# Kernel optimization log

Hardware: AMD Instinct MI355X
Metric: run time of the kernel (lower is better)

The kernel has to match this reference:

```python
import jax, jax.numpy as jnp
import numpy as np

B, T, D, S, K = 8, 4096, 1024, 64, 3
EPS = 1e-5

def setup_inputs() -> dict:
    key = jax.random.key(0)
    ks = jax.random.split(key, 10)
    def lin(k, out_d, in_d):
        s = 1.0 / np.sqrt(in_d)
        return jax.random.uniform(k, (out_d, in_d), jnp.float32, -s, s)
    return {
        "x": jax.random.normal(ks[0], (B, T, D), jnp.float32),
        "norm_w": jnp.ones((D,), jnp.float32),
        "norm_b": jnp.zeros((D,), jnp.float32),
        "in_w": lin(ks[1], 2 * D, D),
        "in_b": jnp.zeros((2 * D,), jnp.float32),
        "conv_w": jax.random.normal(ks[2], (D, 1, K), jnp.float32) / np.sqrt(K),
        "conv_b": jnp.zeros((D,), jnp.float32),
        "dt_w": lin(ks[3], S, D),
        "dt_b": jnp.zeros((S,), jnp.float32),
        "b_w": lin(ks[4], S, D),
        "b_b": jnp.zeros((S,), jnp.float32),
        "c_w": lin(ks[5], S, D),
        "c_b": jnp.zeros((S,), jnp.float32),
        "a_log": jax.random.normal(ks[6], (S,), jnp.float32) * 0.02,
        "d": jnp.ones((D,), jnp.float32),
        "out_w": lin(ks[7], D, D + S),
        "out_b": jnp.zeros((D,), jnp.float32),
    }

def reference(x, norm_w, norm_b, in_w, in_b, conv_w, conv_b,
              dt_w, dt_b, b_w, b_b, c_w, c_b, a_log, d, out_w, out_b):
    bsz, tlen, dim = x.shape
    sdim = a_log.shape[0]
    k = conv_w.shape[-1]
    residual = x
    # LayerNorm
    mu = jnp.mean(x, axis=-1, keepdims=True)
    var = jnp.mean(jnp.square(x - mu), axis=-1, keepdims=True)
    xn = (x - mu) * jax.lax.rsqrt(var + EPS) * norm_w + norm_b
    # in_proj and chunk
    h = xn @ in_w.T + in_b                       # (B,T,2D)
    x_proj, z = jnp.split(h, 2, axis=-1)         # each (B,T,D)
    # depthwise conv over time, 'same' padding
    xc = jax.lax.conv_general_dilated(
        x_proj.transpose(0, 2, 1), conv_w, (1,), [(k // 2, k // 2)],
        dimension_numbers=("NCH", "OIH", "NCH"), feature_group_count=dim)
    x_conv = jnp.tanh((xc + conv_b[None, :, None]).transpose(0, 2, 1))  # (B,T,D)
    # gate projections for all timesteps at once
    dt = jax.nn.softplus(z @ dt_w.T + dt_b) + 1e-4   # (B,T,S)
    b = jnp.tanh(z @ b_w.T + b_b)                    # (B,T,S)
    c = jnp.tanh(z @ c_w.T + c_b)                    # (B,T,S)
    a = -jnp.exp(a_log)                              # (S,)
    decay = jnp.exp(a * dt)                          # (B,T,S)
    # linear recurrence: state_t = state_{t-1} * decay_t + b_t
    def step(state, inp):
        dec_t, b_t = inp
        state = state * dec_t + b_t
        return state, state
    _, states = jax.lax.scan(step, jnp.zeros((bsz, sdim), x.dtype),
                             (decay.transpose(1, 0, 2), b.transpose(1, 0, 2)))
    states = states.transpose(1, 0, 2)               # (B,T,S)
    y = c * states
    mix = jnp.concatenate([x_conv * d, y], axis=-1)  # (B,T,D+S)
    out = mix @ out_w.T + out_b                      # (B,T,D)
    return residual + out
```

## Files before the change

kernel.cpp:

```cpp
#include <hip/hip_runtime.h>

#define TT 4096
#define DD 1024
#define NN 32768

typedef short s16x8 __attribute__((ext_vector_type(8)));
typedef float f32x4 __attribute__((ext_vector_type(4)));
typedef unsigned short ushort_t;

__device__ __forceinline__ unsigned short f2bf(float f) {
  unsigned u = __float_as_uint(f);
  u += 0x7FFFu + ((u >> 16) & 1u);
  return (unsigned short)(u >> 16);
}
__device__ __forceinline__ float bf2f(unsigned short h) {
  return __uint_as_float(((unsigned)h) << 16);
}
__device__ __forceinline__ void load_lds16(const void* g, void* l) {
  __builtin_amdgcn_global_load_lds(
      (const __attribute__((address_space(1))) unsigned int*)g,
      (__attribute__((address_space(3))) unsigned int*)l, 16, 0, 0);
}

__global__ __launch_bounds__(256)
void cvt_kernel(const float* __restrict__ s, ushort_t* __restrict__ d, int n) {
  int i = (blockIdx.x * 256 + threadIdx.x) * 4;
  if (i < n) {
    float4 v = *(const float4*)&s[i];
    ushort4 o; o.x = f2bf(v.x); o.y = f2bf(v.y); o.z = f2bf(v.z); o.w = f2bf(v.w);
    *(ushort4*)&d[i] = o;
  }
}

__global__ __launch_bounds__(256)
void w3pad_kernel(const float* __restrict__ dt_w, const float* __restrict__ b_w,
                  const float* __restrict__ c_w, ushort_t* __restrict__ w3) {
  int e = (blockIdx.x * 256 + threadIdx.x) * 4;
  int row = e >> 10, col = e & 1023;
  float4 v; v.x = 0.f; v.y = 0.f; v.z = 0.f; v.w = 0.f;
  if (row < 64)       v = *(const float4*)&dt_w[(row << 10) + col];
  else if (row < 128) v = *(const float4*)&b_w[((row - 64) << 10) + col];
  else if (row < 192) v = *(const float4*)&c_w[((row - 128) << 10) + col];
  ushort4 o; o.x = f2bf(v.x); o.y = f2bf(v.y); o.z = f2bf(v.z); o.w = f2bf(v.w);
  *(ushort4*)&w3[e] = o;
}

__global__ __launch_bounds__(256)
void ln_kernel(const float* __restrict__ x, const float* __restrict__ w,
               const float* __restrict__ bv, ushort_t* __restrict__ xn)
{
  int row = blockIdx.x * 4 + (threadIdx.x >> 6);
  int lane = threadIdx.x & 63;
  const float* xr = x + (size_t)row * DD;
  float4 v[4];
  float s = 0.f, ss = 0.f;
  #pragma unroll
  for (int j = 0; j < 4; ++j) {
    v[j] = *(const float4*)&xr[j * 256 + lane * 4];
    s  += v[j].x + v[j].y + v[j].z + v[j].w;
    ss += v[j].x * v[j].x + v[j].y * v[j].y + v[j].z * v[j].z + v[j].w * v[j].w;
  }
  #pragma unroll
  for (int off = 32; off > 0; off >>= 1) {
    s  += __shfl_xor(s, off, 64);
    ss += __shfl_xor(ss, off, 64);
  }
  float mean = s * (1.f / 1024.f);
  float var  = ss * (1.f / 1024.f) - mean * mean;
  float rinv = rsqrtf(var + 1e-5f);
  #pragma unroll
  for (int j = 0; j < 4; ++j) {
    int c = j * 256 + lane * 4;
    float4 wv = *(const float4*)&w[c];
    float4 bb = *(const float4*)&bv[c];
    ushort4 o;
    o.x = f2bf((v[j].x - mean) * rinv * wv.x + bb.x);
    o.y = f2bf((v[j].y - mean) * rinv * wv.y + bb.y);
    o.z = f2bf((v[j].z - mean) * rinv * wv.z + bb.z);
    o.w = f2bf((v[j].w - mean) * rinv * wv.w + bb.w);
    *(ushort4*)&xn[(size_t)row * DD + c] = o;
  }
}

template<int EP>
__global__ __launch_bounds__(512, 2)
void gemm256(const ushort_t* __restrict__ A, const ushort_t* __restrict__ W,
             int M, int N, int K,
             const float* __restrict__ bias0,
             ushort_t* __restrict__ o0, ushort_t* __restrict__ o1)
{
  __shared__ ushort_t lds[65536];
  const int tid = threadIdx.x;
  const int lane = tid & 63;
  const int wid = tid >> 6;
  const int wr = wid >> 2;
  const int wc = wid & 3;
  const int lane15 = lane & 15;
  const int lgrp = lane >> 4;
  const int rsw = (lane15 & 7) << 4;
  const int ntn = N >> 8;
  int bid = blockIdx.x;
  { const int cpx = (int)gridDim.x >> 3; bid = (bid & 7) * cpx + (bid >> 3); }
  const int brow = (bid / ntn) << 8;
  const int bcol = (bid % ntn) << 8;
  const int nk = K >> 6;
  const int sRow = tid >> 3;
  const int sCol = (tid & 7) << 4;
  const char* ldsb = (const char*)lds;
  (void)M;

#define STG(bufb, isB, h, kt) do { \
    const int ktc_ = (kt) < nk ? (kt) : nk - 1; \
    const ushort_t* gsrc_ = (isB) ? W : A; \
    const int rowb_ = ((isB) ? bcol : brow) + (h) * 128; \
    _Pragma("unroll") \
    for (int j_ = 0; j_ < 2; ++j_) { \
      const int r_ = j_ * 64 + sRow; \
      load_lds16((const char*)(gsrc_ + (size_t)(rowb_ + r_) * K) + ktc_ * 128 + (sCol ^ ((r_ & 7) << 4)), \
                 (char*)lds + (bufb) * 65536 + (isB) * 32768 + (h) * 16384 + r_ * 128 + sCol); \
    } } while (0)

#define LDA_(bufb, m, kk) \
  (*(const s16x8*)(ldsb + (bufb) * 65536 + wr * 16384 + ((m) * 16 + lane15) * 128 + (((kk) * 64 + lgrp * 16) ^ rsw)))
#define LDB_(bufb, n, kk) \
  (*(const s16x8*)(ldsb + (bufb) * 65536 + 32768 + (wc >> 1) * 16384 + ((wc & 1) * 64 + (n) * 16 + lane15) * 128 + (((kk) * 64 + lgrp * 16) ^ rsw)))

#define BARR() asm volatile("s_barrier" ::: "memory")
#define VMW2() asm volatile("s_waitcnt vmcnt(2)" ::: "memory")
#define VMW4() asm volatile("s_waitcnt vmcnt(4)" ::: "memory")

#define RDA(dst, bufb, mh) do { \
    _Pragma("unroll") for (int kk = 0; kk < 2; ++kk) \
    _Pragma("unroll") for (int q = 0; q < 4; ++q) \
      dst[kk][q] = LDA_(bufb, (mh) * 4 + q, kk); } while (0)
#define RDB(dst, bufb, nh) do { \
    _Pragma("unroll") for (int kk = 0; kk < 2; ++kk) \
    _Pragma("unroll") for (int p = 0; p < 2; ++p) \
      dst[kk][p] = LDB_(bufb, (nh) * 2 + p, kk); } while (0)

#define MFMAQ(AF, BF, mh, nh) do { \
    __builtin_amdgcn_s_setprio(1); \
    _Pragma("unroll") for (int kk = 0; kk < 2; ++kk) \
    _Pragma("unroll") for (int q = 0; q < 4; ++q) \
    _Pragma("unroll") for (int p = 0; p < 2; ++p) \
      acc[(mh) * 4 + q][(nh) * 2 + p] = __builtin_amdgcn_mfma_f32_16x16x32_bf16( \
          AF[kk][q], BF[kk][p], acc[(mh) * 4 + q][(nh) * 2 + p], 0, 0, 0); \
    __builtin_amdgcn_s_setprio(0); } while (0)

  f32x4 acc[8][4];
  #pragma unroll
  for (int m = 0; m < 8; ++m) {
    #pragma unroll
    for (int n = 0; n < 4; ++n) acc[m][n] = (f32x4){0.f, 0.f, 0.f, 0.f};
  }
  s16x8 afP[2][4], afQ[2][4];
  s16x8 b0[2][2], b1[2][2];

  STG(0, 1, 0, 0); STG(0, 0, 0, 0); STG(0, 0, 1, 0); STG(0, 1, 1, 0);
  STG(1, 1, 0, 1); STG(1, 0, 0, 1);
  VMW4(); BARR();
  RDA(afP, 0, 0); RDB(b0, 0, 0);

  const int nIter = nk >> 1;
  for (int it = 0; it < nIter; ++it) {
    const int t0 = 2 * it;
    STG(1, 0, 1, t0 + 1);
    MFMAQ(afP, b0, 0, 0);
    RDB(b1, 0, 1); BARR();
    STG(1, 1, 1, t0 + 1);
    MFMAQ(afP, b1, 0, 1);
    RDA(afQ, 0, 1); BARR();
    STG(0, 1, 0, t0 + 2);
    MFMAQ(afQ, b1, 1, 1);
    VMW2(); BARR();
    STG(0, 0, 0, t0 + 2);
    MFMAQ(afQ, b0, 1, 0);
    RDA(afP, 1, 0); RDB(b1, 1, 1); BARR();
    STG(0, 0, 1, t0 + 2);
    MFMAQ(afP, b1, 0, 1);
    RDB(b0, 1, 0); BARR();
    STG(0, 1, 1, t0 + 2);
    MFMAQ(afP, b0, 0, 0);
    RDA(afQ, 1, 1); BARR();
    STG(1, 1, 0, t0 + 3);
    MFMAQ(afQ, b0, 1, 0);
    VMW2(); BARR();
    STG(1, 0, 0, t0 + 3);
    MFMAQ(afQ, b1, 1, 1);
    RDA(afP, 0, 0); RDB(b0, 0, 0); BARR();
  }
  if (nk & 1) {
    MFMAQ(afP, b0, 0, 0);
    RDB(b1, 0, 1);
    MFMAQ(afP, b1, 0, 1);
    RDA(afQ, 0, 1);
    MFMAQ(afQ, b1, 1, 1);
    MFMAQ(afQ, b0, 1, 0);
  }

#undef STG
#undef LDA_
#undef LDB_
#undef BARR
#undef VMW2
#undef VMW4
#undef RDA
#undef RDB
#undef MFMAQ

  #pragma unroll
  for (int m = 0; m < 8; ++m) {
    #pragma unroll
    for (int i = 0; i < 4; ++i) {
      const int r = brow + wr * 128 + m * 16 + lgrp * 4 + i;
      #pragma unroll
      for (int n = 0; n < 4; ++n) {
        const int col = bcol + wc * 64 + n * 16 + lane15;
        float v = acc[m][n][i] + bias0[col];
        if (col < DD) o0[(size_t)r * DD + col] = f2bf(v);
        else          o1[(size_t)r * DD + (col - DD)] = f2bf(v);
      }
    }
  }
}

__global__ __launch_bounds__(512, 4)
void gemm3_bk32(const ushort_t* __restrict__ A, const ushort_t* __restrict__ W,
                int M, int N, int K,
                const float* __restrict__ bias, const float* __restrict__ resid,
                float* __restrict__ outf)
{
  __shared__ ushort_t lds[24576];
  const int tid = threadIdx.x;
  const int lane = tid & 63;
  const int wid = tid >> 6;
  const int wr = wid >> 2;
  const int wc = wid & 3;
  const int lane15 = lane & 15;
  const int lgrp = lane >> 4;
  const int ntn = N >> 8;
  int bid = blockIdx.x;
  { const int cpx = (int)gridDim.x >> 3; bid = (bid & 7) * cpx + (bid >> 3); }
  const int brow = (bid / ntn) << 7;
  const int bcol = (bid % ntn) << 8;
  const int nk = K >> 5;
  const int sR = tid >> 2;
  const int sC = (tid & 3) << 4;
  const char* ldsb = (const char*)lds;
  (void)M;

  f32x4 acc[4][4];
  #pragma unroll
  for (int q = 0; q < 4; ++q)
    #pragma unroll
    for (int p = 0; p < 4; ++p) acc[q][p] = (f32x4){0.f, 0.f, 0.f, 0.f};

#define STG3(bufb, kt) do { \
    load_lds16((const char*)(A + (size_t)(brow + sR) * K + (kt) * 32) + sC, \
               (char*)lds + (bufb) * 24576 + sR * 64 + sC); \
    load_lds16((const char*)(W + (size_t)(bcol + sR) * K + (kt) * 32) + sC, \
               (char*)lds + (bufb) * 24576 + 8192 + sR * 64 + sC); \
    load_lds16((const char*)(W + (size_t)(bcol + 128 + sR) * K + (kt) * 32) + sC, \
               (char*)lds + (bufb) * 24576 + 8192 + (128 + sR) * 64 + sC); \
  } while (0)

  STG3(0, 0);
  __syncthreads();

  int cur = 0;
  for (int t = 0; t < nk; ++t) {
    if (t + 1 < nk) STG3(cur ^ 1, t + 1);
    s16x8 af[4], bf[4];
    #pragma unroll
    for (int q = 0; q < 4; ++q)
      af[q] = *(const s16x8*)(ldsb + cur * 24576 + (wr * 64 + q * 16 + lane15) * 64 + lgrp * 16);
    #pragma unroll
    for (int p = 0; p < 4; ++p)
      bf[p] = *(const s16x8*)(ldsb + cur * 24576 + 8192 + (wc * 64 + p * 16 + lane15) * 64 + lgrp * 16);
    __builtin_amdgcn_s_setprio(1);
    #pragma unroll
    for (int q = 0; q < 4; ++q)
      #pragma unroll
      for (int p = 0; p < 4; ++p)
        acc[q][p] = __builtin_amdgcn_mfma_f32_16x16x32_bf16(af[q], bf[p], acc[q][p], 0, 0, 0);
    __builtin_amdgcn_s_setprio(0);
    __syncthreads();
    cur ^= 1;
  }
#undef STG3

  #pragma unroll
  for (int q = 0; q < 4; ++q) {
    #pragma unroll
    for (int i = 0; i < 4; ++i) {
      const int r = brow + wr * 64 + q * 16 + lgrp * 4 + i;
      #pragma unroll
      for (int p = 0; p < 4; ++p) {
        const int col = bcol + wc * 64 + p * 16 + lane15;
        outf[(size_t)r * DD + col] = acc[q][p][i] + bias[col] + resid[(size_t)r * DD + col];
      }
    }
  }
}

__global__ __launch_bounds__(256)
void gemm128(const ushort_t* __restrict__ A, const ushort_t* __restrict__ W,
             int M, int N, int K,
             const float* __restrict__ bias0, const float* __restrict__ bias1,
             const float* __restrict__ bias2, const float* __restrict__ alog,
             float* __restrict__ g0, float* __restrict__ g1, float* __restrict__ g2)
{
  __shared__ ushort_t As[128 * 64];
  __shared__ ushort_t Bs[128 * 64];
  const int tid = threadIdx.x;
  const int lane = tid & 63;
  const int wid = tid >> 6;
  const int ntn = N >> 7;
  const int brow = (blockIdx.x / ntn) << 7;
  const int bcol = (blockIdx.x % ntn) << 7;
  const int wr = (wid >> 1) << 6;
  const int wc = (wid & 1) << 6;
  const int lane15 = lane & 15;
  const int lgrp = lane >> 4;
  (void)M;

  f32x4 acc[4][4];
  #pragma unroll
  for (int m = 0; m < 4; ++m)
    #pragma unroll
    for (int n = 0; n < 4; ++n)
      acc[m][n] = (f32x4){0.f, 0.f, 0.f, 0.f};

  const int r0 = tid >> 3;
  const int c0 = (tid & 7) << 3;
  const ushort_t* gA = A + (size_t)(brow + r0) * K + c0;
  const ushort_t* gW = W + (size_t)(bcol + r0) * K + c0;
  ushort_t* lA = &As[r0 * 64 + c0];
  ushort_t* lB = &Bs[r0 * 64 + c0];

  for (int k0 = 0; k0 < K; k0 += 64) {
    #pragma unroll
    for (int j = 0; j < 4; ++j) {
      load_lds16(gA + (size_t)(j * 32) * K + k0, lA + j * 32 * 64);
      load_lds16(gW + (size_t)(j * 32) * K + k0, lB + j * 32 * 64);
    }
    __syncthreads();
    #pragma unroll
    for (int kk = 0; kk < 2; ++kk) {
      s16x8 af[4], bfr[4];
      #pragma unroll
      for (int m = 0; m < 4; ++m)
        af[m] = *(const s16x8*)&As[(wr + m * 16 + lane15) * 64 + kk * 32 + lgrp * 8];
      #pragma unroll
      for (int n = 0; n < 4; ++n)
        bfr[n] = *(const s16x8*)&Bs[(wc + n * 16 + lane15) * 64 + kk * 32 + lgrp * 8];
      #pragma unroll
      for (int m = 0; m < 4; ++m)
        #pragma unroll
        for (int n = 0; n < 4; ++n)
          acc[m][n] = __builtin_amdgcn_mfma_f32_16x16x32_bf16(af[m], bfr[n], acc[m][n], 0, 0, 0);
    }
    __syncthreads();
  }

  #pragma unroll
  for (int m = 0; m < 4; ++m) {
    #pragma unroll
    for (int i = 0; i < 4; ++i) {
      const int r = brow + wr + m * 16 + lgrp * 4 + i;
      #pragma unroll
      for (int n = 0; n < 4; ++n) {
        const int col = bcol + wc + n * 16 + lane15;
        float v = acc[m][n][i];
        if (col < 64) {
          float u = v + bias0[col];
          float sp = (u > 20.f) ? u : log1pf(expf(u));
          float dt = sp + 1e-4f;
          float a = -expf(alog[col]);
          g0[(size_t)r * 64 + col] = expf(a * dt);
        } else if (col < 128) {
          g1[(size_t)r * 64 + (col - 64)] = tanhf(v + bias1[col - 64]);
        } else if (col < 192) {
          g2[(size_t)r * 64 + (col - 128)] = tanhf(v + bias2[col - 128]);
        }
      }
    }
  }
}

__global__ __launch_bounds__(256)
void conv_kernel(const ushort_t* __restrict__ xp, const float* __restrict__ cw,
                 const float* __restrict__ cb, const float* __restrict__ dvec,
                 ushort_t* __restrict__ mix)
{
  int idx = blockIdx.x * 256 + threadIdx.x;
  int row = idx >> 7;
  int d0 = (idx & 127) << 3;
  int t = row & (TT - 1);
  s16x8 cur = *(const s16x8*)&xp[(size_t)row * DD + d0];
  s16x8 prv; s16x8 nxt;
  #pragma unroll
  for (int j = 0; j < 8; ++j) { prv[j] = 0; nxt[j] = 0; }
  if (t > 0)      prv = *(const s16x8*)&xp[(size_t)(row - 1) * DD + d0];
  if (t < TT - 1) nxt = *(const s16x8*)&xp[(size_t)(row + 1) * DD + d0];
  float wv[24];
  #pragma unroll
  for (int j = 0; j < 6; ++j) *(float4*)&wv[j * 4] = *(const float4*)&cw[d0 * 3 + j * 4];
  float cbv[8], dv[8];
  *(float4*)&cbv[0] = *(const float4*)&cb[d0];
  *(float4*)&cbv[4] = *(const float4*)&cb[d0 + 4];
  *(float4*)&dv[0]  = *(const float4*)&dvec[d0];
  *(float4*)&dv[4]  = *(const float4*)&dvec[d0 + 4];
  s16x8 o;
  #pragma unroll
  for (int j = 0; j < 8; ++j) {
    float acc = cbv[j] + bf2f((ushort_t)prv[j]) * wv[j * 3]
              + bf2f((ushort_t)cur[j]) * wv[j * 3 + 1]
              + bf2f((ushort_t)nxt[j]) * wv[j * 3 + 2];
    o[j] = (short)f2bf(tanhf(acc) * dv[j]);
  }
  *(s16x8*)&mix[(size_t)row * 1088 + d0] = o;
}

__global__ void scanA_kernel(const float* __restrict__ dec, const float* __restrict__ bb,
                             float* __restrict__ P, float* __restrict__ Q)
{
  int b = blockIdx.x >> 6, ci = blockIdx.x & 63, s = threadIdx.x;
  size_t base = (((size_t)b * TT) + ci * 64) * 64 + s;
  float p = 1.f, q = 0.f;
  #pragma unroll 4
  for (int t = 0; t < 64; ++t) {
    float d = dec[base + (size_t)t * 64];
    float w = bb[base + (size_t)t * 64];
    q = q * d + w; p *= d;
  }
  int o = (b * 64 + ci) * 64 + s;
  P[o] = p; Q[o] = q;
}

__global__ void scanB_kernel(const float* __restrict__ P, const float* __restrict__ Q,
                             float* __restrict__ I)
{
  int b = blockIdx.x, s = threadIdx.x;
  float st = 0.f;
  for (int ci = 0; ci < 64; ++ci) {
    int o = (b * 64 + ci) * 64 + s;
    I[o] = st;
    st = st * P[o] + Q[o];
  }
}

__global__ void scanC_kernel(const float* __restrict__ dec, const float* __restrict__ bb,
                             const float* __restrict__ cc, const float* __restrict__ I,
                             ushort_t* __restrict__ mix)
{
  int b = blockIdx.x >> 6, ci = blockIdx.x & 63, s = threadIdx.x;
  size_t base = (((size_t)b * TT) + ci * 64) * 64 + s;
  float st = I[(b * 64 + ci) * 64 + s];
  size_t mrow = (size_t)b * TT + ci * 64;
  #pragma unroll 4
  for (int t = 0; t < 64; ++t) {
    size_t o = base + (size_t)t * 64;
    st = st * dec[o] + bb[o];
    mix[(mrow + t) * 1088 + 1024 + s] = (ushort_t)f2bf(cc[o] * st);
  }
}

extern "C" void kernel_launch(void* const* d_in, const int* in_sizes, int n_in,
                              void* d_out, int out_size, void* d_ws, size_t ws_size,
                              hipStream_t stream)
{
  (void)in_sizes; (void)n_in; (void)out_size; (void)ws_size;
  const float* x      = (const float*)d_in[0];
  const float* norm_w = (const float*)d_in[1];
  const float* norm_b = (const float*)d_in[2];
  const float* in_w   = (const float*)d_in[3];
  const float* in_b   = (const float*)d_in[4];
  const float* conv_w = (const float*)d_in[5];
  const float* conv_b = (const float*)d_in[6];
  const float* dt_w   = (const float*)d_in[7];
  const float* dt_b   = (const float*)d_in[8];
  const float* b_w    = (const float*)d_in[9];
  const float* b_b    = (const float*)d_in[10];
  const float* c_w    = (const float*)d_in[11];
  const float* c_b    = (const float*)d_in[12];
  const float* a_log  = (const float*)d_in[13];
  const float* dvec   = (const float*)d_in[14];
  const float* out_w  = (const float*)d_in[15];
  const float* out_b  = (const float*)d_in[16];
  float* out = (float*)d_out;

  char* p = (char*)d_ws;
  ushort_t* mix    = (ushort_t*)p;
  ushort_t* xn     = mix;
  p += 71303168;
  ushort_t* xproj  = (ushort_t*)p; p += 67108864;
  ushort_t* z      = (ushort_t*)p; p += 67108864;
  ushort_t* inw_bf = (ushort_t*)p; p += 4194304;
  ushort_t* w3     = (ushort_t*)p; p += 524288;
  ushort_t* outw_bf= (ushort_t*)p; p += 2228224;
  float* P = (float*)p; p += 131072;
  float* Q = (float*)p; p += 131072;
  float* I = (float*)p; p += 131072;
  float* gdec = (float*)xproj;
  float* gbb  = (float*)((char*)xproj + 8388608);
  float* gcc  = (float*)((char*)xproj + 16777216);

  cvt_kernel<<<2048, 256, 0, stream>>>(in_w,  inw_bf,  2097152);
  cvt_kernel<<<1088, 256, 0, stream>>>(out_w, outw_bf, 1114112);
  w3pad_kernel<<<256, 256, 0, stream>>>(dt_w, b_w, c_w, w3);
  ln_kernel<<<8192, 256, 0, stream>>>(x, norm_w, norm_b, xn);

  gemm256<0><<<(NN / 256) * (2048 / 256), 512, 0, stream>>>(
      xn, inw_bf, NN, 2048, 1024, in_b, xproj, z);

  conv_kernel<<<NN * 128 / 256, 256, 0, stream>>>(xproj, conv_w, conv_b, dvec, mix);

  gemm128<<<(NN / 128) * (256 / 128), 256, 0, stream>>>(
      z, w3, NN, 256, 1024,
      dt_b, b_b, c_b, a_log,
      gdec, gbb, gcc);

  scanA_kernel<<<512, 64, 0, stream>>>(gdec, gbb, P, Q);
  scanB_kernel<<<8, 64, 0, stream>>>(P, Q, I);
  scanC_kernel<<<512, 64, 0, stream>>>(gdec, gbb, gcc, I, mix);

  gemm3_bk32<<<(NN / 128) * (1024 / 256), 512, 0, stream>>>(
      mix, outw_bf, NN, 1024, 1088, out_b, x, out);
}
```

Measured before the change: 441.9 us.

## Fold gate projections into in_proj weights to skip z computation

Precomputes combined gate weights by multiplying the dt/b/c projection weights with the z half of in_proj, plus folded biases. The main in_proj GEMM then only produces x_proj, and the gate GEMM reads the normalized input directly. This removes half of the largest GEMM and the z buffer round trip through memory. In exchange it adds a small per-call weight transpose and GEMM, and changes rounding because folded weights are stored in bf16.

```diff
diff --git a/kernel.cpp b/kernel.cpp
--- a/kernel.cpp
+++ b/kernel.cpp
@@ -43,6 +43,42 @@
   else if (row < 192) v = *(const float4*)&c_w[((row - 128) << 10) + col];
   ushort4 o; o.x = f2bf(v.x); o.y = f2bf(v.y); o.z = f2bf(v.z); o.w = f2bf(v.w);
   *(ushort4*)&w3[e] = o;
+}
+
+__global__ __launch_bounds__(256)
+void tpose_kernel(const float* __restrict__ src, ushort_t* __restrict__ dst) {
+  __shared__ float tile[64][65];
+  int bx = blockIdx.x & 15, by = blockIdx.x >> 4;
+  int tx = threadIdx.x & 63, ty0 = threadIdx.x >> 6;
+  #pragma unroll
+  for (int i = 0; i < 16; ++i) {
+    int ty = ty0 * 16 + i;
+    tile[ty][tx] = src[(size_t)(by * 64 + ty) * 1024 + bx * 64 + tx];
+  }
+  __syncthreads();
+  #pragma unroll
+  for (int i = 0; i < 16; ++i) {
+    int ty = ty0 * 16 + i;
+    dst[(size_t)(bx * 64 + ty) * 1024 + by * 64 + tx] = f2bf(tile[tx][ty]);
+  }
+}
+
+__global__ void gbias_kernel(const float* __restrict__ dt_w, const float* __restrict__ b_w,
+                             const float* __restrict__ c_w, const float* __restrict__ dt_b,
+                             const float* __restrict__ b_b, const float* __restrict__ c_b,
+                             const float* __restrict__ in_b, float* __restrict__ gb) {
+  int i = blockIdx.x, lane = threadIdx.x;
+  const float* wr = i < 64 ? dt_w + (size_t)i * 1024
+                  : i < 128 ? b_w + (size_t)(i - 64) * 1024
+                            : c_w + (size_t)(i - 128) * 1024;
+  float s = 0.f;
+  for (int j = lane; j < 1024; j += 64) s += wr[j] * in_b[1024 + j];
+  #pragma unroll
+  for (int off = 32; off; off >>= 1) s += __shfl_xor(s, off, 64);
+  if (lane == 0) {
+    float bb = i < 64 ? dt_b[i] : i < 128 ? b_b[i - 64] : c_b[i - 128];
+    gb[i] = s + bb;
+  }
 }
 
 __global__ __launch_bounds__(256)
@@ -304,11 +340,8 @@
 }
 
 __global__ __launch_bounds__(256)
-void gemm128(const ushort_t* __restrict__ A, const ushort_t* __restrict__ W,
-             int M, int N, int K,
-             const float* __restrict__ bias0, const float* __restrict__ bias1,
-             const float* __restrict__ bias2, const float* __restrict__ alog,
-             float* __restrict__ g0, float* __restrict__ g1, float* __restrict__ g2)
+void gemm128w(const ushort_t* __restrict__ A, const ushort_t* __restrict__ W,
+              int M, int N, int K, ushort_t* __restrict__ o0)
 {
   __shared__ ushort_t As[128 * 64];
   __shared__ ushort_t Bs[128 * 64];
@@ -371,17 +404,88 @@
       #pragma unroll
       for (int n = 0; n < 4; ++n) {
         const int col = bcol + wc + n * 16 + lane15;
+        o0[(size_t)r * N + col] = f2bf(acc[m][n][i]);
+      }
+    }
+  }
+}
+
+__global__ __launch_bounds__(256)
+void gemm128g(const ushort_t* __restrict__ A, const ushort_t* __restrict__ W,
+              int M, int N, int K,
+              const float* __restrict__ gb, const float* __restrict__ alog,
+              float* __restrict__ g0, float* __restrict__ g1, float* __restrict__ g2)
+{
+  __shared__ ushort_t As[128 * 64];
+  __shared__ ushort_t Bs[128 * 64];
+  const int tid = threadIdx.x;
+  const int lane = tid & 63;
+  const int wid = tid >> 6;
+  const int ntn = N >> 7;
+  const int brow = (blockIdx.x / ntn) << 7;
+  const int bcol = (blockIdx.x % ntn) << 7;
+  const int wr = (wid >> 1) << 6;
+  const int wc = (wid & 1) << 6;
+  const int lane15 = lane & 15;
+  const int lgrp = lane >> 4;
+  (void)M;
+
+  f32x4 acc[4][4];
+  #pragma unroll
+  for (int m = 0; m < 4; ++m)
+    #pragma unroll
+    for (int n = 0; n < 4; ++n)
+      acc[m][n] = (f32x4){0.f, 0.f, 0.f, 0.f};
+
+  const int r0 = tid >> 3;
+  const int c0 = (tid & 7) << 3;
+  const ushort_t* gA = A + (size_t)(brow + r0) * K + c0;
+  const ushort_t* gW = W + (size_t)(bcol + r0) * K + c0;
+  ushort_t* lA = &As[r0 * 64 + c0];
+  ushort_t* lB = &Bs[r0 * 64 + c0];
+
+  for (int k0 = 0; k0 < K; k0 += 64) {
+    #pragma unroll
+    for (int j = 0; j < 4; ++j) {
+      load_lds16(gA + (size_t)(j * 32) * K + k0, lA + j * 32 * 64);
+      load_lds16(gW + (size_t)(j * 32) * K + k0, lB + j * 32 * 64);
+    }
+    __syncthreads();
+    #pragma unroll
+    for (int kk = 0; kk < 2; ++kk) {
+      s16x8 af[4], bfr[4];
+      #pragma unroll
+      for (int m = 0; m < 4; ++m)
+        af[m] = *(const s16x8*)&As[(wr + m * 16 + lane15) * 64 + kk * 32 + lgrp * 8];
+      #pragma unroll
+      for (int n = 0; n < 4; ++n)
+        bfr[n] = *(const s16x8*)&Bs[(wc + n * 16 + lane15) * 64 + kk * 32 + lgrp * 8];
+      #pragma unroll
+      for (int m = 0; m < 4; ++m)
+        #pragma unroll
+        for (int n = 0; n < 4; ++n)
+          acc[m][n] = __builtin_amdgcn_mfma_f32_16x16x32_bf16(af[m], bfr[n], acc[m][n], 0, 0, 0);
+    }
+    __syncthreads();
+  }
+
+  #pragma unroll
+  for (int m = 0; m < 4; ++m) {
+    #pragma unroll
+    for (int i = 0; i < 4; ++i) {
+      const int r = brow + wr + m * 16 + lgrp * 4 + i;
+      #pragma unroll
+      for (int n = 0; n < 4; ++n) {
+        const int col = bcol + wc + n * 16 + lane15;
         float v = acc[m][n][i];
         if (col < 64) {
-          float u = v + bias0[col];
+          float u = v + gb[col];
           float sp = (u > 20.f) ? u : log1pf(expf(u));
-          float dt = sp + 1e-4f;
-          float a = -expf(alog[col]);
-          g0[(size_t)r * 64 + col] = expf(a * dt);
+          g0[(size_t)r * 64 + col] = expf(-expf(alog[col]) * (sp + 1e-4f));
         } else if (col < 128) {
-          g1[(size_t)r * 64 + (col - 64)] = tanhf(v + bias1[col - 64]);
+          g1[(size_t)r * 64 + (col - 64)] = tanhf(v + gb[col]);
         } else if (col < 192) {
-          g2[(size_t)r * 64 + (col - 128)] = tanhf(v + bias2[col - 128]);
+          g2[(size_t)r * 64 + (col - 128)] = tanhf(v + gb[col]);
         }
       }
     }
@@ -495,31 +599,37 @@
   ushort_t* xn     = mix;
   p += 71303168;
   ushort_t* xproj  = (ushort_t*)p; p += 67108864;
-  ushort_t* z      = (ushort_t*)p; p += 67108864;
-  ushort_t* inw_bf = (ushort_t*)p; p += 4194304;
+  char*     zreg   = p;            p += 67108864;
+  ushort_t* w1_bf  = (ushort_t*)p; p += 4194304;
   ushort_t* w3     = (ushort_t*)p; p += 524288;
   ushort_t* outw_bf= (ushort_t*)p; p += 2228224;
   float* P = (float*)p; p += 131072;
   float* Q = (float*)p; p += 131072;
   float* I = (float*)p; p += 131072;
-  float* gdec = (float*)xproj;
-  float* gbb  = (float*)((char*)xproj + 8388608);
-  float* gcc  = (float*)((char*)xproj + 16777216);
-
-  cvt_kernel<<<2048, 256, 0, stream>>>(in_w,  inw_bf,  2097152);
+
+  float* gdec = (float*)zreg;
+  float* gbb  = (float*)(zreg + 8388608);
+  float* gcc  = (float*)(zreg + 16777216);
+  ushort_t* inw2t  = (ushort_t*)(zreg + 33554432);
+  float*    gb     = (float*)(zreg + 37748736);
+  ushort_t* wgates = (ushort_t*)(zreg + 41943040);
+
+  cvt_kernel<<<1024, 256, 0, stream>>>(in_w, w1_bf, 1048576);
   cvt_kernel<<<1088, 256, 0, stream>>>(out_w, outw_bf, 1114112);
+  tpose_kernel<<<256, 256, 0, stream>>>(in_w + 1048576, inw2t);
   w3pad_kernel<<<256, 256, 0, stream>>>(dt_w, b_w, c_w, w3);
+  gemm128w<<<16, 256, 0, stream>>>(w3, inw2t, 256, 1024, 1024, wgates);
+  gbias_kernel<<<192, 64, 0, stream>>>(dt_w, b_w, c_w, dt_b, b_b, c_b, in_b, gb);
+
   ln_kernel<<<8192, 256, 0, stream>>>(x, norm_w, norm_b, xn);
 
-  gemm256<0><<<(NN / 256) * (2048 / 256), 512, 0, stream>>>(
-      xn, inw_bf, NN, 2048, 1024, in_b, xproj, z);
+  gemm256<0><<<(NN / 256) * (1024 / 256), 512, 0, stream>>>(
+      xn, w1_bf, NN, 1024, 1024, in_b, xproj, nullptr);
+
+  gemm128g<<<(NN / 128) * (256 / 128), 256, 0, stream>>>(
+      xn, wgates, NN, 256, 1024, gb, a_log, gdec, gbb, gcc);
 
   conv_kernel<<<NN * 128 / 256, 256, 0, stream>>>(xproj, conv_w, conv_b, dvec, mix);
-
-  gemm128<<<(NN / 128) * (256 / 128), 256, 0, stream>>>(
-      z, w3, NN, 256, 1024,
-      dt_b, b_b, c_b, a_log,
-      gdec, gbb, gcc);
 
   scanA_kernel<<<512, 64, 0, stream>>>(gdec, gbb, P, Q);
   scanB_kernel<<<8, 64, 0, stream>>>(P, Q, I);
```

Measured after the change: 398.0 us. -9.9%, faster.
